# Kernel tuning notes

Measured on AMD Instinct MI355X. Metric: run time of the kernel, lower is better.

The kernel has to match this reference:

```python
import math
import jax, jax.numpy as jnp
import numpy as np

S, R, CM, CZ = 128, 256, 256, 128
H, C, PH, CT, FF = 8, 32, 4, 128, 4
SCALE = 1.0 / math.sqrt(C)


def _ln(x, w, b, eps=1e-5):
    mu = jnp.mean(x, axis=-1, keepdims=True)
    var = jnp.mean((x - mu) ** 2, axis=-1, keepdims=True)
    return (x - mu) * jax.lax.rsqrt(var + eps) * w + b


def _forward(msa, pair, rnm_w, rnm_b, r_gate, r_qkv, r_out, r_bias, cn_w, cn_b, c_gate, c_qkv, c_out, mtn_w, mtn_b, mt_p1, mt_p2, on_w, on_b, o_p1, o_p2, o_out, tmo_n1w, tmo_n1b, tmo_n2w, tmo_n2b, tmo_p1, tmo_p2, tmo_p3, tmo_p4, tmo_p5, tmo_p6, tmi_n1w, tmi_n1b, tmi_n2w, tmi_n2b, tmi_p1, tmi_p2, tmi_p3, tmi_p4, tmi_p5, tmi_p6, tas_nw, tas_nb, tas_gate, tas_qkv, tas_out, tas_bias, tae_nw, tae_nb, tae_gate, tae_qkv, tae_out, tae_bias, ptn_w, ptn_b, pt_p1, pt_p2):
    # --- MSA row attention with pair bias ---
    m = _ln(msa, rnm_w, rnm_b)
    q, k, v = jnp.split(m @ r_qkv, 3, axis=-1)
    q = q.reshape(S, R, H, C); k = k.reshape(S, R, H, C); v = v.reshape(S, R, H, C)
    bias = (pair @ r_bias).transpose(2, 0, 1)  # [H, i, j]
    logits = jnp.einsum('sihc,sjhc->shij', q, k) * SCALE + bias[None]
    o = jnp.einsum('shij,sjhc->sihc', jax.nn.softmax(logits, axis=-1), v).reshape(S, R, CM)
    msa = msa + (jax.nn.sigmoid(m @ r_gate) * o) @ r_out

    # --- MSA column attention (attend over sequence dim per residue) ---
    m = _ln(msa, cn_w, cn_b)
    q, k, v = jnp.split(m @ c_qkv, 3, axis=-1)
    q = q.reshape(S, R, H, C); k = k.reshape(S, R, H, C); v = v.reshape(S, R, H, C)
    logits = jnp.einsum('irhc,jrhc->hrij', q, k) * SCALE
    o = jnp.einsum('hrij,jrhc->irhc', jax.nn.softmax(logits, axis=-1), v).reshape(S, R, CM)
    msa = msa + (jax.nn.sigmoid(m @ c_gate) * o) @ c_out

    # --- MSA transition ---
    m = _ln(msa, mtn_w, mtn_b)
    msa = msa + jax.nn.relu(m @ mt_p1) @ mt_p2

    # --- Outer product mean ---
    m = _ln(msa, on_w, on_b)
    outer = jnp.einsum('sic,sjd->ijcd', m @ o_p1, m @ o_p2) / S
    pair = pair + outer.reshape(R, R, C * C) @ o_out

    # --- Triangle multiplicative update, outgoing (residual on normed pair, as in source) ---
    z = _ln(pair, tmo_n1w, tmo_n1b)
    left = (z @ tmo_p1) * jax.nn.sigmoid(z @ tmo_p2)
    right = (z @ tmo_p3) * jax.nn.sigmoid(z @ tmo_p4)
    g = jax.nn.sigmoid(z @ tmo_p6)
    x = _ln(jnp.einsum('ikc,jkc->ijc', left, right), tmo_n2w, tmo_n2b)
    pair = z + g * (x @ tmo_p5)

    # --- Triangle multiplicative update, incoming ---
    z = _ln(pair, tmi_n1w, tmi_n1b)
    left = (z @ tmi_p1) * jax.nn.sigmoid(z @ tmi_p2)
    right = (z @ tmi_p3) * jax.nn.sigmoid(z @ tmi_p4)
    g = jax.nn.sigmoid(z @ tmi_p6)
    x = _ln(jnp.einsum('kic,kjc->ijc', left, right), tmi_n2w, tmi_n2b)
    pair = z + g * (x @ tmi_p5)

    # --- Triangle attention, starting node: softmax over k of q_ij.k_ik + b_jk ---
    z = _ln(pair, tas_nw, tas_nb)
    b = (z @ tas_bias).transpose(2, 0, 1)  # [h, j, k]
    q, kk, v = jnp.split(z @ tas_qkv, 3, axis=-1)
    q = q.reshape(R, R, PH, C); kk = kk.reshape(R, R, PH, C); v = v.reshape(R, R, PH, C)
    logits = jnp.einsum('ijhc,ikhc->hijk', q, kk) * SCALE + b[:, None]
    o = jnp.einsum('hijk,ikhc->ijhc', jax.nn.softmax(logits, axis=-1), v).reshape(R, R, PH * C)
    pair = z + (jax.nn.sigmoid(z @ tas_gate) * o) @ tas_out

    # --- Triangle attention, ending node: softmax over k of q_ij.k_kj + b_ki ---
    z = _ln(pair, tae_nw, tae_nb)
    b = (z @ tae_bias).transpose(2, 1, 0)  # [h, i, k] = raw[k, i, h]
    q, kk, v = jnp.split(z @ tae_qkv, 3, axis=-1)
    q = q.reshape(R, R, PH, C); kk = kk.reshape(R, R, PH, C); v = v.reshape(R, R, PH, C)
    logits = jnp.einsum('ijhc,kjhc->hijk', q, kk) * SCALE + b[:, :, None, :]
    o = jnp.einsum('hijk,kjhc->ijhc', jax.nn.softmax(logits, axis=-1), v).reshape(R, R, PH * C)
    pair = z + (jax.nn.sigmoid(z @ tae_gate) * o) @ tae_out

    # --- Pair transition ---
    zt = _ln(pair, ptn_w, ptn_b)
    pair = pair + jax.nn.relu(zt @ pt_p1) @ pt_p2

    return (msa, pair)


def setup_inputs() -> dict:
    ks = iter(jax.random.split(jax.random.key(0), 80))
    def n(shape, s=1.0):
        return jax.random.normal(next(ks), shape, dtype=jnp.float32) * s
    w = lambda *shape: n(shape, 0.02)
    ones = lambda d: jnp.ones((d,), jnp.float32)
    zeros = lambda d: jnp.zeros((d,), jnp.float32)
    d = dict(
        msa=n((S, R, CM)), pair=n((R, R, CZ)),
        rnm_w=ones(CM), rnm_b=zeros(CM), r_gate=w(CM, CM), r_qkv=w(CM, 3 * CM), r_out=w(CM, CM), r_bias=w(CZ, H),
        cn_w=ones(CM), cn_b=zeros(CM), c_gate=w(CM, CM), c_qkv=w(CM, 3 * H * C), c_out=w(H * C, CM),
        mtn_w=ones(CM), mtn_b=zeros(CM), mt_p1=w(CM, FF * CM), mt_p2=w(FF * CM, CM),
        on_w=ones(CM), on_b=zeros(CM), o_p1=w(CM, C), o_p2=w(CM, C), o_out=w(C * C, CZ),
        tmo_n1w=ones(CZ), tmo_n1b=zeros(CZ), tmo_n2w=ones(CT), tmo_n2b=zeros(CT),
        tmo_p1=w(CZ, CT), tmo_p2=w(CZ, CT), tmo_p3=w(CZ, CT), tmo_p4=w(CZ, CT), tmo_p5=w(CT, CZ), tmo_p6=w(CZ, CZ),
        tmi_n1w=ones(CZ), tmi_n1b=zeros(CZ), tmi_n2w=ones(CT), tmi_n2b=zeros(CT),
        tmi_p1=w(CZ, CT), tmi_p2=w(CZ, CT), tmi_p3=w(CZ, CT), tmi_p4=w(CZ, CT), tmi_p5=w(CT, CZ), tmi_p6=w(CZ, CZ),
        tas_nw=ones(CZ), tas_nb=zeros(CZ), tas_gate=w(CZ, PH * C), tas_qkv=w(CZ, 3 * PH * C), tas_out=w(PH * C, CZ), tas_bias=w(CZ, PH),
        tae_nw=ones(CZ), tae_nb=zeros(CZ), tae_gate=w(CZ, PH * C), tae_qkv=w(CZ, 3 * PH * C), tae_out=w(PH * C, CZ), tae_bias=w(CZ, PH),
        ptn_w=ones(CZ), ptn_b=zeros(CZ), pt_p1=w(CZ, FF * CZ), pt_p2=w(FF * CZ, CZ),
    )
    return d


def reference(msa, pair, rnm_w, rnm_b, r_gate, r_qkv, r_out, r_bias, cn_w, cn_b, c_gate, c_qkv, c_out, mtn_w, mtn_b, mt_p1, mt_p2, on_w, on_b, o_p1, o_p2, o_out, tmo_n1w, tmo_n1b, tmo_n2w, tmo_n2b, tmo_p1, tmo_p2, tmo_p3, tmo_p4, tmo_p5, tmo_p6, tmi_n1w, tmi_n1b, tmi_n2w, tmi_n2b, tmi_p1, tmi_p2, tmi_p3, tmi_p4, tmi_p5, tmi_p6, tas_nw, tas_nb, tas_gate, tas_qkv, tas_out, tas_bias, tae_nw, tae_nb, tae_gate, tae_qkv, tae_out, tae_bias, ptn_w, ptn_b, pt_p1, pt_p2):
    return _forward(msa, pair, rnm_w, rnm_b, r_gate, r_qkv, r_out, r_bias, cn_w, cn_b, c_gate, c_qkv, c_out, mtn_w, mtn_b, mt_p1, mt_p2, on_w, on_b, o_p1, o_p2, o_out, tmo_n1w, tmo_n1b, tmo_n2w, tmo_n2b, tmo_p1, tmo_p2, tmo_p3, tmo_p4, tmo_p5, tmo_p6, tmi_n1w, tmi_n1b, tmi_n2w, tmi_n2b, tmi_p1, tmi_p2, tmi_p3, tmi_p4, tmi_p5, tmi_p6, tas_nw, tas_nb, tas_gate, tas_qkv, tas_out, tas_bias, tae_nw, tae_nb, tae_gate, tae_qkv, tae_out, tae_bias, ptn_w, ptn_b, pt_p1, pt_p2)
```

## Files before the change

### kernel.cpp

```cpp
#include <hip/hip_runtime.h>
#include <hip/hip_bf16.h>

typedef __hip_bfloat16 bf16;
typedef short v8s __attribute__((ext_vector_type(8)));
typedef float v4f __attribute__((ext_vector_type(4)));

#define SCALE_ 0.17677669529663687f
#define LOG2E_ 1.4426950408889634f

static __device__ __forceinline__ float sigf(float x){ return 1.f / (1.f + expf(-x)); }
static __device__ __forceinline__ float tof(float x){ return x; }
static __device__ __forceinline__ float tof(bf16 x){ return __bfloat162float(x); }
template<typename T> static __device__ __forceinline__ T fromf(float x);
template<> __device__ __forceinline__ float fromf<float>(float x){ return x; }
template<> __device__ __forceinline__ bf16  fromf<bf16 >(float x){ return __float2bfloat16(x); }
static __device__ __forceinline__ short b2s(float x){ bf16 b = __float2bfloat16(x); return *(short*)&b; }
static __device__ __forceinline__ float s2f(unsigned short s){ return __uint_as_float((unsigned)s << 16); }

static __device__ __forceinline__ void gload16(const void* g, void* l){
    __builtin_amdgcn_global_load_lds(
        (const __attribute__((address_space(1))) void*)g,
        (__attribute__((address_space(3))) void*)l,
        16, 0, 0);
}
static __device__ __forceinline__ v8s swzread(const short* S, int R, int l4){
    return *(const v8s*)&S[(R << 5) + (((l4) ^ (R & 3)) << 3)];
}

__global__ void detect_kernel(const unsigned short* w, int* flag){
    if (blockIdx.x == 0 && threadIdx.x == 0) flag[0] = (w[0] == 0x3F80) ? 0 : 1;
}
struct WC  { const void* s; bf16* d; int n; };
struct WC56 { WC w[56]; };
__global__ void cvtall_kernel(WC56 a, const int* flag){
    WC W = a.w[blockIdx.y];
    int i = blockIdx.x*256 + threadIdx.x;
    if (i >= W.n) return;
    float v = flag[0] ? ((const float*)W.s)[i] : tof(((const bf16*)W.s)[i]);
    W.d[i] = fromf<bf16>(v);
}
struct TC4 { const void* s; bf16* d; int K, N; };
struct TC34 { TC4 w[34]; };
__global__ void cvtTall_kernel(TC34 a, const int* flag){
    TC4 W = a.w[blockIdx.y];
    int idx = blockIdx.x*256 + threadIdx.x;
    if (idx >= W.K*W.N) return;
    int k = idx / W.N, n = idx - k*W.N;
    float v = flag[0] ? ((const float*)W.s)[idx] : tof(((const bf16*)W.s)[idx]);
    W.d[(size_t)n*W.K + k] = fromf<bf16>(v);
}
__global__ void cvt2f_kernel(const void* src, float* dst, int n4, const int* flag){
    int i = blockIdx.x*256 + threadIdx.x;
    if (i >= n4) return;
    if (flag[0]) ((float4*)dst)[i] = ((const float4*)src)[i];
    else {
        ushort4 v = ((const ushort4*)src)[i];
        float4 o;
        o.x = s2f(v.x); o.y = s2f(v.y); o.z = s2f(v.z); o.w = s2f(v.w);
        ((float4*)dst)[i] = o;
    }
}

template<typename TIN, typename TOUT, int D>
__global__ __launch_bounds__(256) void ln_kernel(const TIN* x, const bf16* w, const bf16* b, TOUT* y){
    constexpr int E = D/64;
    int wave = threadIdx.x >> 6, lane = threadIdx.x & 63;
    int row = blockIdx.x*4 + wave;
    size_t base = (size_t)row * D + lane*E;
    float v[E];
    if constexpr (sizeof(TIN)==4){
        if constexpr (E==4){ float4 t = *(const float4*)((const float*)x+base); v[0]=t.x;v[1]=t.y;v[2]=t.z;v[3]=t.w; }
        else { float2 t = *(const float2*)((const float*)x+base); v[0]=t.x;v[1]=t.y; }
    } else {
        if constexpr (E==4){ ushort4 t = *(const ushort4*)((const ushort*)x+base); v[0]=s2f(t.x);v[1]=s2f(t.y);v[2]=s2f(t.z);v[3]=s2f(t.w); }
        else { ushort2 t = *(const ushort2*)((const ushort*)x+base); v[0]=s2f(t.x);v[1]=s2f(t.y); }
    }
    float s1=0.f, s2=0.f;
    #pragma unroll
    for (int j=0;j<E;j++){ s1 += v[j]; s2 += v[j]*v[j]; }
    #pragma unroll
    for (int m=1;m<64;m<<=1){ s1 += __shfl_xor(s1,m,64); s2 += __shfl_xor(s2,m,64); }
    float mu  = s1*(1.0f/D);
    float var = s2*(1.0f/D) - mu*mu;
    float rs  = rsqrtf(fmaxf(var, 0.f) + 1e-5f);
    ushort wv[E], bw[E];
    if constexpr (E==4){ *(ushort4*)wv = *(const ushort4*)((const ushort*)w + lane*4);
                         *(ushort4*)bw = *(const ushort4*)((const ushort*)b + lane*4); }
    else               { *(ushort2*)wv = *(const ushort2*)((const ushort*)w + lane*2);
                         *(ushort2*)bw = *(const ushort2*)((const ushort*)b + lane*2); }
    ushort o[E];
    #pragma unroll
    for (int j=0;j<E;j++) o[j] = (ushort)b2s((v[j]-mu)*rs*s2f(wv[j]) + s2f(bw[j]));
    if constexpr (E==4) *(ushort4*)((ushort*)y + base) = *(ushort4*)o;
    else                *(ushort2*)((ushort*)y + base) = *(ushort2*)o;
}
template<int D>
__global__ __launch_bounds__(256) void ln2_kernel(const float* x, const bf16* w, const bf16* b, float* y, bf16* yB){
    constexpr int E = D/64;
    int wave = threadIdx.x >> 6, lane = threadIdx.x & 63;
    int row = blockIdx.x*4 + wave;
    size_t base = (size_t)row * D + lane*E;
    float2 t = *(const float2*)(x+base);
    float v0 = t.x, v1 = t.y;
    float s1 = v0+v1, s2 = v0*v0+v1*v1;
    #pragma unroll
    for (int m=1;m<64;m<<=1){ s1 += __shfl_xor(s1,m,64); s2 += __shfl_xor(s2,m,64); }
    float mu  = s1*(1.0f/D);
    float var = s2*(1.0f/D) - mu*mu;
    float rs  = rsqrtf(fmaxf(var, 0.f) + 1e-5f);
    ushort2 wv = *(const ushort2*)((const ushort*)w + lane*2);
    ushort2 bw = *(const ushort2*)((const ushort*)b + lane*2);
    float o0 = (v0-mu)*rs*s2f(wv.x) + s2f(bw.x);
    float o1 = (v1-mu)*rs*s2f(wv.y) + s2f(bw.y);
    float2 of; of.x = o0; of.y = o1;
    *(float2*)(y+base) = of;
    ushort ob[2]; ob[0] = (ushort)b2s(o0); ob[1] = (ushort)b2s(o1);
    *(ushort2*)((ushort*)yB + base) = *(ushort2*)ob;
}
__global__ __launch_bounds__(256) void lnT256_kernel(const float* x, const bf16* w, const bf16* b, bf16* y, bf16* yT){
    int wave = threadIdx.x >> 6, lane = threadIdx.x & 63;
    int row = blockIdx.x*4 + wave;
    int s = row >> 8, r = row & 255;
    size_t base = (size_t)row * 256 + lane*4;
    float4 t = *(const float4*)(x+base);
    float v[4] = {t.x, t.y, t.z, t.w};
    float s1=0.f, s2=0.f;
    #pragma unroll
    for (int j=0;j<4;j++){ s1 += v[j]; s2 += v[j]*v[j]; }
    #pragma unroll
    for (int m=1;m<64;m<<=1){ s1 += __shfl_xor(s1,m,64); s2 += __shfl_xor(s2,m,64); }
    float mu  = s1*(1.0f/256);
    float var = s2*(1.0f/256) - mu*mu;
    float rs  = rsqrtf(fmaxf(var, 0.f) + 1e-5f);
    ushort4 wv = *(const ushort4*)((const ushort*)w + lane*4);
    ushort4 bw = *(const ushort4*)((const ushort*)b + lane*4);
    ushort o[4];
    o[0] = (ushort)b2s((v[0]-mu)*rs*s2f(wv.x) + s2f(bw.x));
    o[1] = (ushort)b2s((v[1]-mu)*rs*s2f(wv.y) + s2f(bw.y));
    o[2] = (ushort)b2s((v[2]-mu)*rs*s2f(wv.z) + s2f(bw.z));
    o[3] = (ushort)b2s((v[3]-mu)*rs*s2f(wv.w) + s2f(bw.w));
    *(ushort4*)((ushort*)y + base) = *(ushort4*)o;
    *(ushort4*)((ushort*)yT + (((size_t)r << 7) + s)*256 + lane*4) = *(ushort4*)o;
}
__global__ __launch_bounds__(256) void ln2T128_kernel(const float* x, const bf16* w, const bf16* b,
                               float* y, bf16* yB, bf16* yT){
    int wave = threadIdx.x >> 6, lane = threadIdx.x & 63;
    int row = blockIdx.x*4 + wave;
    int i = row >> 8, j = row & 255;
    size_t base = (size_t)row * 128 + lane*2;
    float2 t = *(const float2*)(x+base);
    float v0 = t.x, v1 = t.y;
    float s1 = v0+v1, s2 = v0*v0+v1*v1;
    #pragma unroll
    for (int m=1;m<64;m<<=1){ s1 += __shfl_xor(s1,m,64); s2 += __shfl_xor(s2,m,64); }
    float mu  = s1*(1.0f/128);
    float var = s2*(1.0f/128) - mu*mu;
    float rs  = rsqrtf(fmaxf(var, 0.f) + 1e-5f);
    ushort2 wv = *(const ushort2*)((const ushort*)w + lane*2);
    ushort2 bw = *(const ushort2*)((const ushort*)b + lane*2);
    float o0 = (v0-mu)*rs*s2f(wv.x) + s2f(bw.x);
    float o1 = (v1-mu)*rs*s2f(wv.y) + s2f(bw.y);
    float2 of; of.x = o0; of.y = o1;
    *(float2*)(y+base) = of;
    ushort ob[2]; ob[0] = (ushort)b2s(o0); ob[1] = (ushort)b2s(o1);
    *(ushort2*)((ushort*)yB + base) = *(ushort2*)ob;
    *(ushort2*)((ushort*)yT + (((size_t)j << 8) + i)*128 + lane*2) = *(ushort2*)ob;
}

template<typename TC, typename TD>
__global__ __launch_bounds__(256) void mgemm_kernel(
    const bf16* A, const bf16* Wt, const TC* Cadd, TD* D,
    int M, int N, int K, int relu)
{
    __shared__ short As[4096];
    __shared__ short Bs[4096];
    int t = threadIdx.x;
    int wave = t >> 6, lane = t & 63;
    int wm = (wave >> 1) * 64, wn = (wave & 1) * 64;
    int m0 = blockIdx.y * 128, n0 = blockIdx.x * 128;
    const int l15 = lane & 15, l4 = lane >> 4;
    const int p0 = t, p1 = 256 + t;
    const int r0s = p0 >> 2, q0s = (p0 & 3) ^ (r0s & 3);
    const int r1s = p1 >> 2, q1s = (p1 & 3) ^ (r1s & 3);

// ... 30 lines not shown
            int col = n0 + wn + nf*16 + l15;
            #pragma unroll
            for (int r=0; r<4; r++){
                int row = r0 + r;
                float v = acc[mf][nf][r];
                if (Cadd) v += tof(Cadd[(size_t)row*N + col]);
                if (relu) v = fmaxf(v, 0.f);
                D[(size_t)row*N + col] = fromf<TD>(v);
            }
        }
    }
}

template<typename TA>
__global__ __launch_bounds__(256) void mgemm64_kernel(
    const TA* A, const bf16* Wt, bf16* D, int M, int N, int K)
{
    __shared__ short As[128][40];
    __shared__ short Bs[64][40];
    int t = threadIdx.x;
    int wave = t >> 6, lane = t & 63;
    int wm = (wave >> 1) * 64, wn = (wave & 1) * 32;
    int m0 = blockIdx.y * 128;
    int srow = t >> 1, skh = (t & 1) * 16;
    const int l15 = lane & 15, l4 = lane >> 4;

    v4f acc[4][2];
    #pragma unroll
    for (int i=0;i<4;i++){ acc[i][0] = (v4f)0.f; acc[i][1] = (v4f)0.f; }

    for (int k0 = 0; k0 < K; k0 += 32){
        if constexpr (sizeof(TA) == 2){
            const ushort* ag = (const ushort*)A + (size_t)(m0 + srow)*K + k0 + skh;
            *(uint4*)&As[srow][skh]     = *(const uint4*)(ag);
            *(uint4*)&As[srow][skh + 8] = *(const uint4*)(ag + 8);
        } else {
            const float* ap = (const float*)A + (size_t)(m0 + srow)*K + k0 + skh;
            #pragma unroll
            for (int q = 0; q < 4; q++){
                float4 v = *(const float4*)(ap + q*4);
                As[srow][skh+q*4+0] = b2s(v.x); As[srow][skh+q*4+1] = b2s(v.y);
                As[srow][skh+q*4+2] = b2s(v.z); As[srow][skh+q*4+3] = b2s(v.w);
            }
        }
        if (srow < 64){
            if (srow < N){
                const ushort* wg = (const ushort*)Wt + (size_t)srow*K + k0 + skh;
                *(uint4*)&Bs[srow][skh]     = *(const uint4*)(wg);
                *(uint4*)&Bs[srow][skh + 8] = *(const uint4*)(wg + 8);
            } else {
                uint4 z = {0,0,0,0};
                *(uint4*)&Bs[srow][skh] = z; *(uint4*)&Bs[srow][skh + 8] = z;
            }
        }
        __syncthreads();
        v8s af[4], bfr[2];
        #pragma unroll
        for (int mf=0; mf<4; mf++) af[mf] = *(const v8s*)&As[wm + mf*16 + l15][l4*8];
        #pragma unroll
        for (int nf=0; nf<2; nf++) bfr[nf] = *(const v8s*)&Bs[wn + nf*16 + l15][l4*8];
        #pragma unroll
        for (int mf=0; mf<4; mf++)
            #pragma unroll
            for (int nf=0; nf<2; nf++)
                acc[mf][nf] = __builtin_amdgcn_mfma_f32_16x16x32_bf16(
                    af[mf], bfr[nf], acc[mf][nf], 0, 0, 0);
        __syncthreads();
    }
    #pragma unroll
    for (int mf=0; mf<4; mf++){
        int r0 = m0 + wm + mf*16 + l4*4;
        #pragma unroll
        for (int nf=0; nf<2; nf++){
            int col = wn + nf*16 + l15;
            if (col < N){
                #pragma unroll
                for (int r=0; r<4; r++)
                    D[(size_t)(r0+r)*N + col] = fromf<bf16>(acc[mf][nf][r]);
            }
        }
    }
}

__global__ __launch_bounds__(256) void mgemm_opmA_kernel(
    const bf16* G, const bf16* Wt, const float* Cadd, float* D, int M, int N, int K)
{
    __shared__ short As[4096];
    __shared__ short Bs[4096];
    int t = threadIdx.x;
    int wave = t >> 6, lane = t & 63;
    int wm = (wave >> 1) * 64, wn = (wave & 1) * 64;
    int m0 = blockIdx.y * 128, n0 = blockIdx.x * 128;
    const int l15 = lane & 15, l4 = lane >> 4;
    const int p0 = t, p1 = 256 + t;
    const int r0s = p0 >> 2, q0s = (p0 & 3) ^ (r0s & 3);
    const int r1s = p1 >> 2, q1s = (p1 & 3) ^ (r1s & 3);
    const int ma = m0 + r0s, mb = m0 + r1s;

    v4f acc[4][4];
    #pragma unroll
    for (int i=0;i<4;i++)
        #pragma unroll
        for(int j=0;j<4;j++) acc[i][j] = (v4f)0.f;

    for (int k0 = 0; k0 < K; k0 += 32){
        int kb5 = k0 >> 5;
        gload16((const ushort*)G + ((size_t)((ma>>8)*32 + kb5))*8192 + (ma&255)*32 + q0s*8, &As[p0*8]);
        gload16((const ushort*)G + ((size_t)((mb>>8)*32 + kb5))*8192 + (mb&255)*32 + q1s*8, &As[p1*8]);
        gload16((const ushort*)Wt + (size_t)(n0 + r0s)*K + k0 + q0s*8, &Bs[p0*8]);
        gload16((const ushort*)Wt + (size_t)(n0 + r1s)*K + k0 + q1s*8, &Bs[p1*8]);
        __syncthreads();
        v8s af[4], bfr[4];
        #pragma unroll
        for (int mf=0; mf<4; mf++) af[mf]  = swzread(As, wm + mf*16 + l15, l4);
        #pragma unroll
        for (int nf=0; nf<4; nf++) bfr[nf] = swzread(Bs, wn + nf*16 + l15, l4);
        #pragma unroll
        for (int mf=0; mf<4; mf++)
            #pragma unroll
            for (int nf=0; nf<4; nf++)
                acc[mf][nf] = __builtin_amdgcn_mfma_f32_16x16x32_bf16(
                    af[mf], bfr[nf], acc[mf][nf], 0, 0, 0);
        __syncthreads();
    }
    #pragma unroll
    for (int mf=0; mf<4; mf++){
        int r0 = m0 + wm + mf*16 + l4*4;
        #pragma unroll
        for (int nf=0; nf<4; nf++){
            int col = n0 + wn + nf*16 + l15;
            #pragma unroll
            for (int r=0; r<4; r++){
                size_t idx = (size_t)(r0+r)*N + col;
                D[idx] = Cadd[idx] + acc[mf][nf][r];
            }
        }
    }
}

__global__ __launch_bounds__(256) void mgemm_gated_kernel(
    const bf16* G, const bf16* Oo, const bf16* Wt, const float* Cadd, float* D,
    int M, int N, int K)
{
    __shared__ short As[128][40];
    __shared__ short Bs[4096];
    int t = threadIdx.x;
    int wave = t >> 6, lane = t & 63;
    int wm = (wave >> 1) * 64, wn = (wave & 1) * 64;
    int m0 = blockIdx.y * 128, n0 = blockIdx.x * 128;
    int srow = t >> 1, skh = (t & 1) * 16;
    const int l15 = lane & 15, l4 = lane >> 4;
    const int p0 = t, p1 = 256 + t;
    const int r0s = p0 >> 2, q0s = (p0 & 3) ^ (r0s & 3);
    const int r1s = p1 >> 2, q1s = (p1 & 3) ^ (r1s & 3);

    v4f acc[4][4];
    #pragma unroll
    for (int i=0;i<4;i++)
        #pragma unroll
        for(int j=0;j<4;j++) acc[i][j] = (v4f)0.f;

    for (int k0 = 0; k0 < K; k0 += 32){
        gload16((const ushort*)Wt + (size_t)(n0 + r0s)*K + k0 + q0s*8, &Bs[p0*8]);
        gload16((const ushort*)Wt + (size_t)(n0 + r1s)*K + k0 + q1s*8, &Bs[p1*8]);
        const ushort* gg = (const ushort*)G  + (size_t)(m0 + srow)*K + k0 + skh;
        const ushort* oo = (const ushort*)Oo + (size_t)(m0 + srow)*K + k0 + skh;
        ushort ga[16], oa[16];
        *(uint4*)ga = *(const uint4*)gg;   *(uint4*)(ga+8) = *(const uint4*)(gg+8);
        *(uint4*)oa = *(const uint4*)oo;   *(uint4*)(oa+8) = *(const uint4*)(oo+8);
        #pragma unroll
        for (int j = 0; j < 16; j++)
            As[srow][skh + j] = b2s(s2f(oa[j]) * sigf(s2f(ga[j])));
        __syncthreads();
        v8s af[4], bfr[4];
        #pragma unroll
        for (int mf=0; mf<4; mf++) af[mf]  = *(const v8s*)&As[wm + mf*16 + l15][l4*8];
        #pragma unroll
        for (int nf=0; nf<4; nf++) bfr[nf] = swzread(Bs, wn + nf*16 + l15, l4);
        #pragma unroll
        for (int mf=0; mf<4; mf++)
            #pragma unroll
            for (int nf=0; nf<4; nf++)
                acc[mf][nf] = __builtin_amdgcn_mfma_f32_16x16x32_bf16(
                    af[mf], bfr[nf], acc[mf][nf], 0, 0, 0);
        __syncthreads();
    }
    #pragma unroll
    for (int mf=0; mf<4; mf++){
        int r0 = m0 + wm + mf*16 + l4*4;
        #pragma unroll
        for (int nf=0; nf<4; nf++){
            int col = n0 + wn + nf*16 + l15;
            #pragma unroll
            for (int r=0; r<4; r++){
                int row = r0 + r;
                float v = acc[mf][nf][r];
                if (Cadd) v += Cadd[(size_t)row*N + col];
                D[(size_t)row*N + col] = v;
            }
        }
    }
}

__global__ __launch_bounds__(256) void mgemm_glu_kernel(
    const bf16* A, const bf16* W1t, const bf16* W2t, bf16* D,
    int M, int N, int K)
{
    __shared__ short As[4096];
    __shared__ short B1s[4096];
    __shared__ short B2s[4096];
    int t = threadIdx.x;
    int wave = t >> 6, lane = t & 63;
    int wm = (wave >> 1) * 64, wn = (wave & 1) * 64;
    int m0 = blockIdx.y * 128, n0 = blockIdx.x * 128;
    const int l15 = lane & 15, l4 = lane >> 4;
    const int p0 = t, p1 = 256 + t;
    const int r0s = p0 >> 2, q0s = (p0 & 3) ^ (r0s & 3);
    const int r1s = p1 >> 2, q1s = (p1 & 3) ^ (r1s & 3);

    v4f acc1[4][4], acc2[4][4];
    #pragma unroll
    for (int i=0;i<4;i++)
        #pragma unroll
        for(int j=0;j<4;j++){ acc1[i][j] = (v4f)0.f; acc2[i][j] = (v4f)0.f; }

    for (int k0 = 0; k0 < K; k0 += 32){
        gload16((const ushort*)A   + (size_t)(m0 + r0s)*K + k0 + q0s*8, &As[p0*8]);
        gload16((const ushort*)A   + (size_t)(m0 + r1s)*K + k0 + q1s*8, &As[p1*8]);
        gload16((const ushort*)W1t + (size_t)(n0 + r0s)*K + k0 + q0s*8, &B1s[p0*8]);
        gload16((const ushort*)W1t + (size_t)(n0 + r1s)*K + k0 + q1s*8, &B1s[p1*8]);
        gload16((const ushort*)W2t + (size_t)(n0 + r0s)*K + k0 + q0s*8, &B2s[p0*8]);
        gload16((const ushort*)W2t + (size_t)(n0 + r1s)*K + k0 + q1s*8, &B2s[p1*8]);
        __syncthreads();
        v8s af[4], b1[4], b2[4];
        #pragma unroll
        for (int mf=0; mf<4; mf++) af[mf] = swzread(As, wm + mf*16 + l15, l4);
        #pragma unroll
        for (int nf=0; nf<4; nf++){
            b1[nf] = swzread(B1s, wn + nf*16 + l15, l4);
            b2[nf] = swzread(B2s, wn + nf*16 + l15, l4);
        }
        #pragma unroll
        for (int mf=0; mf<4; mf++)
            #pragma unroll
            for (int nf=0; nf<4; nf++){
                acc1[mf][nf] = __builtin_amdgcn_mfma_f32_16x16x32_bf16(af[mf], b1[nf], acc1[mf][nf], 0,0,0);
                acc2[mf][nf] = __builtin_amdgcn_mfma_f32_16x16x32_bf16(af[mf], b2[nf], acc2[mf][nf], 0,0,0);
            }
        __syncthreads();
    }
    #pragma unroll
    for (int mf=0; mf<4; mf++){
        int r0 = m0 + wm + mf*16 + l4*4;
        #pragma unroll
        for (int nf=0; nf<4; nf++){
            int col = n0 + wn + nf*16 + l15;
            #pragma unroll
            for (int r=0; r<4; r++)
                D[(size_t)(r0+r)*N + col] = fromf<bf16>(acc1[mf][nf][r] * sigf(acc2[mf][nf][r]));
        }
    }
}

__global__ __launch_bounds__(256) void mgemm_pairgate_kernel(
    const bf16* A, const bf16* Wt, const bf16* G, float* P,
    int M, int N, int K)
{
    __shared__ short As[4096];
    __shared__ short Bs[4096];
    int t = threadIdx.x;
    int wave = t >> 6, lane = t & 63;
    int wm = (wave >> 1) * 64, wn = (wave & 1) * 64;
    int m0 = blockIdx.y * 128, n0 = blockIdx.x * 128;
    const int l15 = lane & 15, l4 = lane >> 4;
    const int p0 = t, p1 = 256 + t;
    const int r0s = p0 >> 2, q0s = (p0 & 3) ^ (r0s & 3);
    const int r1s = p1 >> 2, q1s = (p1 & 3) ^ (r1s & 3);

    v4f acc[4][4];
    #pragma unroll
    for (int i=0;i<4;i++)
        #pragma unroll
        for(int j=0;j<4;j++) acc[i][j] = (v4f)0.f;

    for (int k0 = 0; k0 < K; k0 += 32){
        gload16((const ushort*)A  + (size_t)(m0 + r0s)*K + k0 + q0s*8, &As[p0*8]);
        gload16((const ushort*)A  + (size_t)(m0 + r1s)*K + k0 + q1s*8, &As[p1*8]);
        gload16((const ushort*)Wt + (size_t)(n0 + r0s)*K + k0 + q0s*8, &Bs[p0*8]);
        gload16((const ushort*)Wt + (size_t)(n0 + r1s)*K + k0 + q1s*8, &Bs[p1*8]);
        __syncthreads();
        v8s af[4], bfr[4];
        #pragma unroll
        for (int mf=0; mf<4; mf++) af[mf]  = swzread(As, wm + mf*16 + l15, l4);
        #pragma unroll
        for (int nf=0; nf<4; nf++) bfr[nf] = swzread(Bs, wn + nf*16 + l15, l4);
        #pragma unroll
        for (int mf=0; mf<4; mf++)
            #pragma unroll
            for (int nf=0; nf<4; nf++)
                acc[mf][nf] = __builtin_amdgcn_mfma_f32_16x16x32_bf16(
                    af[mf], bfr[nf], acc[mf][nf], 0, 0, 0);
        __syncthreads();
    }
    #pragma unroll
    for (int mf=0; mf<4; mf++){
        int r0 = m0 + wm + mf*16 + l4*4;
        #pragma unroll
        for (int nf=0; nf<4; nf++){
            int col = n0 + wn + nf*16 + l15;
            #pragma unroll
            for (int r=0; r<4; r++){
                size_t idx = (size_t)(r0+r)*N + col;
                P[idx] += sigf(tof(G[idx])) * acc[mf][nf][r];
            }
        }
    }
}

__global__ __launch_bounds__(256) void bmgemm_kernel(
    const bf16* A_, const bf16* Wt_, bf16* D_)
{
    const int K = 256, N = 256;
    const bf16* A  = A_  + (size_t)blockIdx.z*65536;
    const bf16* Wt = Wt_ + (size_t)blockIdx.z*65536;
    bf16*       D  = D_  + (size_t)blockIdx.z*65536;
    __shared__ short As[4096];
    __shared__ short Bs[4096];
    int t = threadIdx.x;
    int wave = t >> 6, lane = t & 63;
    int wm = (wave >> 1) * 64, wn = (wave & 1) * 64;
    int m0 = blockIdx.y * 128, n0 = blockIdx.x * 128;
    const int l15 = lane & 15, l4 = lane >> 4;
    const int p0 = t, p1 = 256 + t;
    const int r0s = p0 >> 2, q0s = (p0 & 3) ^ (r0s & 3);
    const int r1s = p1 >> 2, q1s = (p1 & 3) ^ (r1s & 3);

    v4f acc[4][4];
    #pragma unroll
    for (int i=0;i<4;i++)
        #pragma unroll
        for(int j=0;j<4;j++) acc[i][j] = (v4f)0.f;

// ... 84 lines not shown
        const ushort* bbase = (const ushort*)Bp + (size_t)h*65536;
        #pragma unroll
        for (int r = 0; r < 4; r++){
            const ushort* bp = bbase + (size_t)(q0 + wq + l4*4 + r)*256 + l15*16;
            *(uint4*)&bv[r][0] = *(const uint4*)(bp);
            *(uint4*)&bv[r][8] = *(const uint4*)(bp + 8);
        }
    }
    __syncthreads();

    v4f sacc[NF];
    #pragma unroll
    for (int f = 0; f < NF; f++){
        v8s bk_ = *(const v8s*)&Ks[(f*16+l15)*KST + l4*8];
        sacc[f] = __builtin_amdgcn_mfma_f32_16x16x32_bf16(aq, bk_, (v4f)0.f, 0, 0, 0);
    }
    float mrow[4] = {-3e38f,-3e38f,-3e38f,-3e38f};
    #pragma unroll
    for (int f = 0; f < NF; f++){
        #pragma unroll
        for (int r = 0; r < 4; r++){
            float v = sacc[f][r]*scale;
            if (Bp) v += s2f(bv[r][f]);
            sacc[f][r] = v;
            mrow[r] = fmaxf(mrow[r], v);
        }
    }
    #pragma unroll
    for (int m = 1; m < 16; m <<= 1){
        #pragma unroll
        for (int r = 0; r < 4; r++) mrow[r] = fmaxf(mrow[r], __shfl_xor(mrow[r], m, 64));
    }
    float srow[4] = {0.f,0.f,0.f,0.f};
    #pragma unroll
    for (int f = 0; f < NF; f++)
        #pragma unroll
        for (int r = 0; r < 4; r++){
            float e = exp2f(sacc[f][r] - mrow[r]);
            sacc[f][r] = e; srow[r] += e;
        }
    #pragma unroll
    for (int m = 1; m < 16; m <<= 1){
        #pragma unroll
        for (int r = 0; r < 4; r++) srow[r] += __shfl_xor(srow[r], m, 64);
    }
    float inv[4];
    #pragma unroll
    for (int r = 0; r < 4; r++) inv[r] = 1.f / srow[r];

    __syncthreads();
    const int PB = wave*16*PST;
    #pragma unroll
    for (int f = 0; f < NF; f++)
        #pragma unroll
        for (int r = 0; r < 4; r++)
            Ps[PB + (l4*4+r)*PST + f*16 + l15] = b2s(sacc[f][r]);
    v4f oacc0 = (v4f)0.f, oacc1 = (v4f)0.f;
    #pragma unroll
    for (int kk = 0; kk < KL; kk++){
        v8s ap   = *(const v8s*)&Ps[PB + l15*PST + kk*32 + l4*8];
        v8s bvv0 = *(const v8s*)&vbuf[l15*PST + kk*32 + l4*8];
        v8s bvv1 = *(const v8s*)&vbuf[(16+l15)*PST + kk*32 + l4*8];
        oacc0 = __builtin_amdgcn_mfma_f32_16x16x32_bf16(ap, bvv0, oacc0, 0, 0, 0);
        oacc1 = __builtin_amdgcn_mfma_f32_16x16x32_bf16(ap, bvv1, oacc1, 0, 0, 0);
    }
    #pragma unroll
    for (int r = 0; r < 4; r++){
        long long qg = q0 + wq + l4*4 + r;
        O[(long long)b*ob + qg*oq + h*32 + l15]      = fromf<bf16>(oacc0[r]*inv[r]);
        O[(long long)b*ob + qg*oq + h*32 + 16 + l15] = fromf<bf16>(oacc1[r]*inv[r]);
    }
}

__global__ void opm_T2_kernel(const bf16* src, bf16* aT, bf16* bT){
    int idx = blockIdx.x*256 + threadIdx.x;
    if (idx >= 2097152) return;
    int half = idx >> 20; int e = idx & 1048575;
    int s = e >> 13; int rem = e & 8191; int i = rem >> 5; int c = rem & 31;
    bf16 v = src[((size_t)s*256 + i)*64 + half*32 + c];
    if (half == 0) aT[((size_t)(i*32+c))*128 + s] = fromf<bf16>(tof(v) * (1.0f/128.0f));
    else           bT[((size_t)(i*32+c))*128 + s] = v;
}

__global__ __launch_bounds__(256) void triT_fwd_kernel(const bf16* in, bf16* out, int swap){
    __shared__ bf16 tile[32][34];
    int i  = blockIdx.z;
    int k0 = blockIdx.x*32;
    int c0 = blockIdx.y*32;
    int tx = threadIdx.x & 31, ty = threadIdx.x >> 5;
    for (int kk = ty; kk < 32; kk += 8){
        int k = k0+kk;
        size_t src = swap ? ((size_t)(k*256+i)*128 + c0+tx) : ((size_t)(i*256+k)*128 + c0+tx);
        tile[kk][tx] = in[src];
    }
    __syncthreads();
    for (int cc = ty; cc < 32; cc += 8){
        out[((size_t)(c0+cc)*256 + i)*256 + k0+tx] = tile[tx][cc];
    }
}
__global__ __launch_bounds__(256) void triT_bwd_kernel(const bf16* in, bf16* out){
    __shared__ bf16 tile[32][34];
    int i  = blockIdx.z;
    int j0 = blockIdx.x*32;
    int c0 = blockIdx.y*32;
    int tx = threadIdx.x & 31, ty = threadIdx.x >> 5;
    for (int cc = ty; cc < 32; cc += 8){
        tile[cc][tx] = in[((size_t)(c0+cc)*256 + i)*256 + j0+tx];
    }
    __syncthreads();
    for (int jj = ty; jj < 32; jj += 8){
        out[((size_t)i*256 + j0+jj)*128 + c0+tx] = tile[tx][jj];
    }
}

extern "C" void kernel_launch(void* const* d_in, const int* in_sizes, int n_in,
                              void* d_out, int out_size, void* d_ws, size_t ws_size,
                              hipStream_t stream) {
    (void)n_in; (void)out_size; (void)ws_size;
    const int NM = 8388608;
    const int NP = 8388608;

    float* msaF  = (float*)d_out;
    float* pairF = msaF + NM;

    char* w8 = (char*)d_ws;
    bf16*  B0 = (bf16*)(w8 + 0);
    bf16*  B1 = (bf16*)(w8 + 16777216);
    bf16*  B2 = (bf16*)(w8 + 33554432);
    bf16*  B5 = (bf16*)(w8 + 50331648);
    bf16*  B6 = (bf16*)(w8 + 67108864);
    bf16*  B4 = (bf16*)(w8 + 117440512);
    bf16*  BP = (bf16*)(w8 + 118489088);
    bf16*  Wb = (bf16*)(w8 + 119537664);
    bf16*  WtP= (bf16*)(w8 + 123731968);
    int*   flag = (int*)(w8 + 127926272);

    dim3 b256(256);
    auto nb = [](int n){ return (n + 255)/256; };
    const float SC2 = SCALE_ * LOG2E_;

    detect_kernel<<<1, 1, 0, stream>>>((const unsigned short*)d_in[2], flag);
    bf16* cw[58];
    WC56 wcArr;
    int maxN = 0;
    { size_t off = 0;
      for (int i = 2; i < 58; i++){
          cw[i] = Wb + off; off += (size_t)in_sizes[i];
          wcArr.w[i-2] = { d_in[i], cw[i], in_sizes[i] };
          if (in_sizes[i] > maxN) maxN = in_sizes[i];
      } }
    cvtall_kernel<<<dim3(nb(maxN), 56), b256, 0, stream>>>(wcArr, flag);

    struct TWh { int idx, K, N; };
    const TWh tw[34] = {{4,256,256},{5,256,768},{6,256,256},{7,128,8},
        {10,256,256},{11,256,768},{12,256,256},
        {15,256,1024},{16,1024,256},{19,256,32},{20,256,32},{21,1024,128},
        {26,128,128},{27,128,128},{28,128,128},{29,128,128},{30,128,128},{31,128,128},
        {36,128,128},{37,128,128},{38,128,128},{39,128,128},{40,128,128},{41,128,128},
        {44,128,128},{45,128,384},{46,128,128},{47,128,4},
        {50,128,128},{51,128,384},{52,128,128},{53,128,4},
        {56,128,512},{57,512,128}};
    bf16* cwT[58] = {};
    TC34 tcArr;
    int maxKN = 0;
    { size_t off = 0;
      for (int wi = 0; wi < 34; wi++){
          const TWh& w = tw[wi];
          cwT[w.idx] = WtP + off; off += (size_t)w.K * w.N;
          tcArr.w[wi] = { d_in[w.idx], cwT[w.idx], w.K, w.N };
          if (w.K*w.N > maxKN) maxKN = w.K*w.N;
      } }
    cvtTall_kernel<<<dim3(nb(maxKN), 34), b256, 0, stream>>>(tcArr, flag);

    cvt2f_kernel<<<nb(NM/4), b256, 0, stream>>>(d_in[0], msaF,  NM/4, flag);
    cvt2f_kernel<<<nb(NP/4), b256, 0, stream>>>(d_in[1], pairF, NP/4, flag);

    const bf16 *rnm_w=cw[2],  *rnm_b=cw[3];
    const bf16 *cn_w=cw[8],   *cn_b=cw[9];
    const bf16 *mtn_w=cw[13], *mtn_b=cw[14];
    const bf16 *on_w=cw[17],  *on_b=cw[18];
    const bf16 *tmo_n1w=cw[22],*tmo_n1b=cw[23],*tmo_n2w=cw[24],*tmo_n2b=cw[25];
    const bf16 *tmi_n1w=cw[32],*tmi_n1b=cw[33],*tmi_n2w=cw[34],*tmi_n2b=cw[35];
    const bf16 *tas_nw=cw[42],*tas_nb=cw[43];
    const bf16 *tae_nw=cw[48],*tae_nb=cw[49];
    const bf16 *ptn_w=cw[54], *ptn_b=cw[55];

    auto mg_b = [&](const bf16* A, const bf16* Wt, bf16* Dd, int M,int N,int K,int relu){
        dim3 g(N/128, M/128);
        mgemm_kernel<float,bf16><<<g, b256, 0, stream>>>(A, Wt, (const float*)nullptr, Dd, M,N,K,relu);
    };
    auto mg_f = [&](const bf16* A, const bf16* Wt, const float* Cs, float* Dd, int M,int N,int K){
        dim3 g(N/128, M/128);
        mgemm_kernel<float,float><<<g, b256, 0, stream>>>(A, Wt, Cs, Dd, M,N,K,0);
    };
    auto mg_gated = [&](const bf16* G, const bf16* Oo, const bf16* Wt, float* Dd, int M,int N,int K){
        dim3 g(N/128, M/128);
        mgemm_gated_kernel<<<g, b256, 0, stream>>>(G, Oo, Wt, Dd, Dd, M,N,K);
    };
    auto mg_glu = [&](const bf16* A, const bf16* W1, const bf16* W2, bf16* Dd, int M,int N,int K){
        dim3 g(N/128, M/128);
        mgemm_glu_kernel<<<g, b256, 0, stream>>>(A, W1, W2, Dd, M,N,K);
    };
    auto mg64_b = [&](const bf16* A, const bf16* Wt, bf16* Dd, int M,int N,int K){
        dim3 g(1, M/128);
        mgemm64_kernel<bf16><<<g, b256, 0, stream>>>(A, Wt, Dd, M,N,K);
    };
    auto mg64_f = [&](const float* A, const bf16* Wt, bf16* Dd, int M,int N,int K){
        dim3 g(1, M/128);
        mgemm64_kernel<float><<<g, b256, 0, stream>>>(A, Wt, Dd, M,N,K);
    };

    ln_kernel<float,bf16,256><<<8192, 256, 0, stream>>>(msaF, rnm_w, rnm_b, B0);
    mg_b(B0, cwT[4], B1, 32768, 256, 256, 0);
    mg64_f(pairF, cwT[7], B4, 65536, 8, 128);
    biasperm_kernel<<<nb(524288), b256, 0, stream>>>(B4, BP, 8, 0);
    mg_b(B0, cwT[5], B6, 32768, 768, 256, 0);
    fattn_kernel<256><<<dim3(128,8,4), b256, 0, stream>>>(
        B6, B6+256, B6+512, BP, B2,
        196608, 768, 196608, 768,  65536, 256, SC2);
    mg_gated(B1, B2, cwT[6], msaF, 32768, 256, 256);

    lnT256_kernel<<<8192, 256, 0, stream>>>(msaF, cn_w, cn_b, B0, B2);
    mg_b(B0, cwT[10], B1, 32768, 256, 256, 0);
    mg_b(B2, cwT[11], B6, 32768, 768, 256, 0);
    fattn_kernel<128><<<dim3(256,8,2), b256, 0, stream>>>(
        B6, B6+256, B6+512, nullptr, B0,
        98304, 768, 98304, 768,  256, 65536, SC2);
    mg_gated(B1, B0, cwT[12], msaF, 32768, 256, 256);

    ln_kernel<float,bf16,256><<<8192, 256, 0, stream>>>(msaF, mtn_w, mtn_b, B0);
    for (int q = 0; q < 2; q++){
        size_t off = (size_t)q * 16384 * 256;
        mg_b(B0 + off, cwT[15], B6, 16384, 1024, 256, 1);
        mg_f(B6, cwT[16], msaF + off, msaF + off, 16384, 256, 1024);
    }

    ln_kernel<float,bf16,256><<<8192, 256, 0, stream>>>(msaF, on_w, on_b, B0);
    mg64_b(B0, cwT[19], B1, 32768, 64, 256);
    opm_T2_kernel<<<nb(2097152), b256, 0, stream>>>(B1, B6, B6 + 1048576);
    for (int ic = 0; ic < 8; ic++){
        mg_b(B6 + (size_t)ic*131072, B6 + 1048576, B0, 1024, 8192, 128, 0);
        dim3 g(1, 64);
        mgemm_opmA_kernel<<<g, b256, 0, stream>>>(B0, cwT[21],
            pairF + (size_t)ic*1048576, pairF + (size_t)ic*1048576, 8192, 128, 1024);
    }

    ln2_kernel<128><<<16384, 256, 0, stream>>>(pairF, tmo_n1w, tmo_n1b, pairF, B5);
    mg_glu(B5, cwT[26], cwT[27], B2, 65536, 128, 128);
    mg_glu(B5, cwT[28], cwT[29], B0, 65536, 128, 128);
    triT_fwd_kernel<<<dim3(8,4,256), b256, 0, stream>>>(B2, B1, 0);
    triT_fwd_kernel<<<dim3(8,4,256), b256, 0, stream>>>(B0, B2, 0);
    bmgemm_kernel<<<dim3(2,2,128), b256, 0, stream>>>(B1, B2, B0);
    triT_bwd_kernel<<<dim3(8,4,256), b256, 0, stream>>>(B0, B1);
    ln_kernel<bf16,bf16,128><<<16384, 256, 0, stream>>>(B1, tmo_n2w, tmo_n2b, B1);
    mg_b(B5, cwT[31], B0, 65536, 128, 128, 0);
    { dim3 g(1, 512);
      mgemm_pairgate_kernel<<<g, b256, 0, stream>>>(B1, cwT[30], B0, pairF, 65536, 128, 128); }

    ln2_kernel<128><<<16384, 256, 0, stream>>>(pairF, tmi_n1w, tmi_n1b, pairF, B5);
    mg_glu(B5, cwT[36], cwT[37], B2, 65536, 128, 128);
    mg_glu(B5, cwT[38], cwT[39], B0, 65536, 128, 128);
    triT_fwd_kernel<<<dim3(8,4,256), b256, 0, stream>>>(B2, B1, 1);
    triT_fwd_kernel<<<dim3(8,4,256), b256, 0, stream>>>(B0, B2, 1);
    bmgemm_kernel<<<dim3(2,2,128), b256, 0, stream>>>(B1, B2, B0);
    triT_bwd_kernel<<<dim3(8,4,256), b256, 0, stream>>>(B0, B1);
    ln_kernel<bf16,bf16,128><<<16384, 256, 0, stream>>>(B1, tmi_n2w, tmi_n2b, B1);
    mg_b(B5, cwT[41], B0, 65536, 128, 128, 0);
    { dim3 g(1, 512);
      mgemm_pairgate_kernel<<<g, b256, 0, stream>>>(B1, cwT[40], B0, pairF, 65536, 128, 128); }

    ln2_kernel<128><<<16384, 256, 0, stream>>>(pairF, tas_nw, tas_nb, pairF, B5);
    mg64_b(B5, cwT[47], B4, 65536, 4, 128);
    biasperm_kernel<<<nb(262144), b256, 0, stream>>>(B4, BP, 4, 0);
    mg_b(B5, cwT[44], B1, 65536, 128, 128, 0);
    mg_b(B5, cwT[45], B6, 65536, 384, 128, 0);
    fattn_kernel<256><<<dim3(256,4,4), b256, 0, stream>>>(
        B6, B6+128, B6+256, BP, B2,
        98304, 384, 98304, 384,  32768, 128, SC2);
    mg_gated(B1, B2, cwT[46], pairF, 65536, 128, 128);

    ln2T128_kernel<<<16384, 256, 0, stream>>>(pairF, tae_nw, tae_nb, pairF, B5, B2);
    mg64_b(B5, cwT[53], B4, 65536, 4, 128);
    biasperm_kernel<<<nb(262144), b256, 0, stream>>>(B4, BP, 4, 1);
    mg_b(B5, cwT[50], B1, 65536, 128, 128, 0);
    mg_b(B2, cwT[51], B6, 65536, 384, 128, 0);
    fattn_kernel<256><<<dim3(256,4,4), b256, 0, stream>>>(
        B6, B6+128, B6+256, BP, B2,
        98304, 384, 98304, 384,  128, 32768, SC2);
    mg_gated(B1, B2, cwT[52], pairF, 65536, 128, 128);

    ln_kernel<float,bf16,128><<<16384, 256, 0, stream>>>(pairF, ptn_w, ptn_b, B0);
    for (int q = 0; q < 2; q++){
        size_t off = (size_t)q * 32768 * 128;
        mg_b(B0 + off, cwT[56], B6, 32768, 512, 128, 1);
        mg_f(B6, cwT[57], pairF + off, pairF + off, 32768, 128, 512);
    }
}
```

Baseline: 1.806 ms.

## Batch outer-product-mean and triangle GEMMs into fewer multi-job launches

The outer-product-mean chunk loop now issues its two GEMMs four chunks at a time through blockIdx.z, using four scratch buffers. The two GLU projections and the plain gate projection of each triangle update are merged into one three-job launch, and the two transposes are merged into one. This cuts kernel launch count and raises grid occupancy for small launches. The cost is extra scratch memory (B6 offsets) and per-block branching on job mode.

```diff
diff --git a/kernel.cpp b/kernel.cpp
--- a/kernel.cpp
+++ b/kernel.cpp
@@ -96,10 +96,9 @@
 }
 template<int D>
 __global__ __launch_bounds__(256) void ln2_kernel(const float* x, const bf16* w, const bf16* b, float* y, bf16* yB){
-    constexpr int E = D/64;
     int wave = threadIdx.x >> 6, lane = threadIdx.x & 63;
     int row = blockIdx.x*4 + wave;
-    size_t base = (size_t)row * D + lane*E;
+    size_t base = (size_t)row * D + lane*2;
     float2 t = *(const float2*)(x+base);
     float v0 = t.x, v1 = t.y;
     float s1 = v0+v1, s2 = v0*v0+v1*v1;
@@ -296,9 +295,68 @@
     }
 }
 
-__global__ __launch_bounds__(256) void mgemm_opmA_kernel(
-    const bf16* G, const bf16* Wt, const float* Cadd, float* D, int M, int N, int K)
+struct P4 { bf16* p[4]; };
+__global__ __launch_bounds__(256) void mgemm_opmG_kernel(
+    const bf16* aT, const bf16* bT, P4 dst, int icbase)
 {
+    const int N = 8192, K = 128;
+    const bf16* A = aT + (size_t)(icbase + blockIdx.z)*131072;
+    bf16* D = dst.p[blockIdx.z];
+    __shared__ short As[4096];
+    __shared__ short Bs[4096];
+    int t = threadIdx.x;
+    int wave = t >> 6, lane = t & 63;
+    int wm = (wave >> 1) * 64, wn = (wave & 1) * 64;
+    int m0 = blockIdx.y * 128, n0 = blockIdx.x * 128;
+    const int l15 = lane & 15, l4 = lane >> 4;
+    const int p0 = t, p1 = 256 + t;
+    const int r0s = p0 >> 2, q0s = (p0 & 3) ^ (r0s & 3);
+    const int r1s = p1 >> 2, q1s = (p1 & 3) ^ (r1s & 3);
+
+    v4f acc[4][4];
+    #pragma unroll
+    for (int i=0;i<4;i++)
+        #pragma unroll
+        for(int j=0;j<4;j++) acc[i][j] = (v4f)0.f;
+
+    for (int k0 = 0; k0 < K; k0 += 32){
+        gload16((const ushort*)A  + (size_t)(m0 + r0s)*K + k0 + q0s*8, &As[p0*8]);
+        gload16((const ushort*)A  + (size_t)(m0 + r1s)*K + k0 + q1s*8, &As[p1*8]);
+        gload16((const ushort*)bT + (size_t)(n0 + r0s)*K + k0 + q0s*8, &Bs[p0*8]);
+        gload16((const ushort*)bT + (size_t)(n0 + r1s)*K + k0 + q1s*8, &Bs[p1*8]);
+        __syncthreads();
+        v8s af[4], bfr[4];
+        #pragma unroll
+        for (int mf=0; mf<4; mf++) af[mf]  = swzread(As, wm + mf*16 + l15, l4);
+        #pragma unroll
+        for (int nf=0; nf<4; nf++) bfr[nf] = swzread(Bs, wn + nf*16 + l15, l4);
+        #pragma unroll
+        for (int mf=0; mf<4; mf++)
+            #pragma unroll
+            for (int nf=0; nf<4; nf++)
+                acc[mf][nf] = __builtin_amdgcn_mfma_f32_16x16x32_bf16(
+                    af[mf], bfr[nf], acc[mf][nf], 0, 0, 0);
+        __syncthreads();
+    }
+    #pragma unroll
+    for (int mf=0; mf<4; mf++){
+        int r0 = m0 + wm + mf*16 + l4*4;
+        #pragma unroll
+        for (int nf=0; nf<4; nf++){
+            int col = n0 + wn + nf*16 + l15;
+            #pragma unroll
+            for (int r=0; r<4; r++)
+                D[(size_t)(r0 + r)*N + col] = fromf<bf16>(acc[mf][nf][r]);
+        }
+    }
+}
+
+__global__ __launch_bounds__(256) void mgemm_opmA4_kernel(
+    P4 gsrc, const bf16* Wt, float* pairBase, int icbase)
+{
+    const int N = 128, K = 1024;
+    const bf16* G = gsrc.p[blockIdx.z];
+    float* D = pairBase + (size_t)(icbase + blockIdx.z)*1048576;
     __shared__ short As[4096];
     __shared__ short Bs[4096];
     int t = threadIdx.x;
@@ -346,7 +404,7 @@
             #pragma unroll
             for (int r=0; r<4; r++){
                 size_t idx = (size_t)(r0+r)*N + col;
-                D[idx] = Cadd[idx] + acc[mf][nf][r];
+                D[idx] = D[idx] + acc[mf][nf][r];
             }
         }
     }
@@ -416,13 +474,14 @@
     }
 }
 
-__global__ __launch_bounds__(256) void mgemm_glu_kernel(
-    const bf16* A, const bf16* W1t, const bf16* W2t, bf16* D,
-    int M, int N, int K)
+struct GluJob { const bf16* W1; const bf16* W2; bf16* D; int mode; };
+__global__ __launch_bounds__(256) void mgemm_glu3_kernel(
+    const bf16* A, GluJob j0, GluJob j1, GluJob j2, int M, int N, int K)
 {
     __shared__ short As[4096];
     __shared__ short B1s[4096];
     __shared__ short B2s[4096];
+    GluJob J = (blockIdx.z == 0) ? j0 : ((blockIdx.z == 1) ? j1 : j2);
     int t = threadIdx.x;
     int wave = t >> 6, lane = t & 63;
     int wm = (wave >> 1) * 64, wn = (wave & 1) * 64;
@@ -439,28 +498,35 @@
         for(int j=0;j<4;j++){ acc1[i][j] = (v4f)0.f; acc2[i][j] = (v4f)0.f; }
 
     for (int k0 = 0; k0 < K; k0 += 32){
-        gload16((const ushort*)A   + (size_t)(m0 + r0s)*K + k0 + q0s*8, &As[p0*8]);
-        gload16((const ushort*)A   + (size_t)(m0 + r1s)*K + k0 + q1s*8, &As[p1*8]);
-        gload16((const ushort*)W1t + (size_t)(n0 + r0s)*K + k0 + q0s*8, &B1s[p0*8]);
-        gload16((const ushort*)W1t + (size_t)(n0 + r1s)*K + k0 + q1s*8, &B1s[p1*8]);
-        gload16((const ushort*)W2t + (size_t)(n0 + r0s)*K + k0 + q0s*8, &B2s[p0*8]);
-        gload16((const ushort*)W2t + (size_t)(n0 + r1s)*K + k0 + q1s*8, &B2s[p1*8]);
-        __syncthreads();
-        v8s af[4], b1[4], b2[4];
+        gload16((const ushort*)A    + (size_t)(m0 + r0s)*K + k0 + q0s*8, &As[p0*8]);
+        gload16((const ushort*)A    + (size_t)(m0 + r1s)*K + k0 + q1s*8, &As[p1*8]);
+        gload16((const ushort*)J.W1 + (size_t)(n0 + r0s)*K + k0 + q0s*8, &B1s[p0*8]);
+        gload16((const ushort*)J.W1 + (size_t)(n0 + r1s)*K + k0 + q1s*8, &B1s[p1*8]);
+        if (J.mode == 0){
+            gload16((const ushort*)J.W2 + (size_t)(n0 + r0s)*K + k0 + q0s*8, &B2s[p0*8]);
+            gload16((const ushort*)J.W2 + (size_t)(n0 + r1s)*K + k0 + q1s*8, &B2s[p1*8]);
+        }
+        __syncthreads();
+        v8s af[4], b1[4];
         #pragma unroll
         for (int mf=0; mf<4; mf++) af[mf] = swzread(As, wm + mf*16 + l15, l4);
         #pragma unroll
-        for (int nf=0; nf<4; nf++){
-            b1[nf] = swzread(B1s, wn + nf*16 + l15, l4);
-            b2[nf] = swzread(B2s, wn + nf*16 + l15, l4);
-        }
+        for (int nf=0; nf<4; nf++) b1[nf] = swzread(B1s, wn + nf*16 + l15, l4);
         #pragma unroll
         for (int mf=0; mf<4; mf++)
             #pragma unroll
-            for (int nf=0; nf<4; nf++){
+            for (int nf=0; nf<4; nf++)
                 acc1[mf][nf] = __builtin_amdgcn_mfma_f32_16x16x32_bf16(af[mf], b1[nf], acc1[mf][nf], 0,0,0);
-                acc2[mf][nf] = __builtin_amdgcn_mfma_f32_16x16x32_bf16(af[mf], b2[nf], acc2[mf][nf], 0,0,0);
-            }
+        if (J.mode == 0){
+            v8s b2[4];
+            #pragma unroll
+            for (int nf=0; nf<4; nf++) b2[nf] = swzread(B2s, wn + nf*16 + l15, l4);
+            #pragma unroll
+            for (int mf=0; mf<4; mf++)
+                #pragma unroll
+                for (int nf=0; nf<4; nf++)
+                    acc2[mf][nf] = __builtin_amdgcn_mfma_f32_16x16x32_bf16(af[mf], b2[nf], acc2[mf][nf], 0,0,0);
+        }
         __syncthreads();
     }
     #pragma unroll
@@ -470,8 +536,11 @@
         for (int nf=0; nf<4; nf++){
             int col = n0 + wn + nf*16 + l15;
             #pragma unroll
-            for (int r=0; r<4; r++)
-                D[(size_t)(r0+r)*N + col] = fromf<bf16>(acc1[mf][nf][r] * sigf(acc2[mf][nf][r]));
+            for (int r=0; r<4; r++){
+                float v = acc1[mf][nf][r];
+                if (J.mode == 0) v *= sigf(acc2[mf][nf][r]);
+                J.D[(size_t)(r0+r)*N + col] = fromf<bf16>(v);
+            }
         }
     }
 }
@@ -722,9 +791,14 @@
     else           bT[((size_t)(i*32+c))*128 + s] = v;
 }
 
-__global__ __launch_bounds__(256) void triT_fwd_kernel(const bf16* in, bf16* out, int swap){
+__global__ __launch_bounds__(256) void triT_fwd2_kernel(
+    const bf16* in0, bf16* out0, const bf16* in1, bf16* out1, int swap)
+{
     __shared__ bf16 tile[32][34];
-    int i  = blockIdx.z;
+    int zz = blockIdx.z;
+    int i  = zz & 255;
+    const bf16* in = (zz < 256) ? in0 : in1;
+    bf16* out      = (zz < 256) ? out0 : out1;
     int k0 = blockIdx.x*32;
     int c0 = blockIdx.y*32;
     int tx = threadIdx.x & 31, ty = threadIdx.x >> 5;
@@ -837,10 +911,6 @@
         dim3 g(N/128, M/128);
         mgemm_gated_kernel<<<g, b256, 0, stream>>>(G, Oo, Wt, Dd, Dd, M,N,K);
     };
-    auto mg_glu = [&](const bf16* A, const bf16* W1, const bf16* W2, bf16* Dd, int M,int N,int K){
-        dim3 g(N/128, M/128);
-        mgemm_glu_kernel<<<g, b256, 0, stream>>>(A, W1, W2, Dd, M,N,K);
-    };
     auto mg64_b = [&](const bf16* A, const bf16* Wt, bf16* Dd, int M,int N,int K){
         dim3 g(1, M/128);
         mgemm64_kernel<bf16><<<g, b256, 0, stream>>>(A, Wt, Dd, M,N,K);
@@ -878,36 +948,35 @@
     ln_kernel<float,bf16,256><<<8192, 256, 0, stream>>>(msaF, on_w, on_b, B0);
     mg64_b(B0, cwT[19], B1, 32768, 64, 256);
     opm_T2_kernel<<<nb(2097152), b256, 0, stream>>>(B1, B6, B6 + 1048576);
-    for (int ic = 0; ic < 8; ic++){
-        mg_b(B6 + (size_t)ic*131072, B6 + 1048576, B0, 1024, 8192, 128, 0);
-        dim3 g(1, 64);
-        mgemm_opmA_kernel<<<g, b256, 0, stream>>>(B0, cwT[21],
-            pairF + (size_t)ic*1048576, pairF + (size_t)ic*1048576, 8192, 128, 1024);
-    }
+    { P4 g; g.p[0] = B0; g.p[1] = B1; g.p[2] = B2; g.p[3] = B5;
+      for (int icb = 0; icb < 8; icb += 4){
+          mgemm_opmG_kernel<<<dim3(64,8,4), b256, 0, stream>>>(B6, B6 + 1048576, g, icb);
+          mgemm_opmA4_kernel<<<dim3(1,64,4), b256, 0, stream>>>(g, cwT[21], pairF, icb);
+      } }
 
     ln2_kernel<128><<<16384, 256, 0, stream>>>(pairF, tmo_n1w, tmo_n1b, pairF, B5);
-    mg_glu(B5, cwT[26], cwT[27], B2, 65536, 128, 128);
-    mg_glu(B5, cwT[28], cwT[29], B0, 65536, 128, 128);
-    triT_fwd_kernel<<<dim3(8,4,256), b256, 0, stream>>>(B2, B1, 0);
-    triT_fwd_kernel<<<dim3(8,4,256), b256, 0, stream>>>(B0, B2, 0);
-    bmgemm_kernel<<<dim3(2,2,128), b256, 0, stream>>>(B1, B2, B0);
+    { GluJob j0 = {cwT[26], cwT[27], B2, 0};
+      GluJob j1 = {cwT[28], cwT[29], B0, 0};
+      GluJob j2 = {cwT[31], cwT[31], B6, 1};
+      mgemm_glu3_kernel<<<dim3(1,512,3), b256, 0, stream>>>(B5, j0, j1, j2, 65536, 128, 128); }
+    triT_fwd2_kernel<<<dim3(8,4,512), b256, 0, stream>>>(B2, B1, B0, B6 + 8388608, 0);
+    bmgemm_kernel<<<dim3(2,2,128), b256, 0, stream>>>(B1, B6 + 8388608, B0);
     triT_bwd_kernel<<<dim3(8,4,256), b256, 0, stream>>>(B0, B1);
     ln_kernel<bf16,bf16,128><<<16384, 256, 0, stream>>>(B1, tmo_n2w, tmo_n2b, B1);
-    mg_b(B5, cwT[31], B0, 65536, 128, 128, 0);
     { dim3 g(1, 512);
-      mgemm_pairgate_kernel<<<g, b256, 0, stream>>>(B1, cwT[30], B0, pairF, 65536, 128, 128); }
+      mgemm_pairgate_kernel<<<g, b256, 0, stream>>>(B1, cwT[30], B6, pairF, 65536, 128, 128); }
 
     ln2_kernel<128><<<16384, 256, 0, stream>>>(pairF, tmi_n1w, tmi_n1b, pairF, B5);
-    mg_glu(B5, cwT[36], cwT[37], B2, 65536, 128, 128);
-    mg_glu(B5, cwT[38], cwT[39], B0, 65536, 128, 128);
-    triT_fwd_kernel<<<dim3(8,4,256), b256, 0, stream>>>(B2, B1, 1);
-    triT_fwd_kernel<<<dim3(8,4,256), b256, 0, stream>>>(B0, B2, 1);
-    bmgemm_kernel<<<dim3(2,2,128), b256, 0, stream>>>(B1, B2, B0);
+    { GluJob j0 = {cwT[36], cwT[37], B2, 0};
+      GluJob j1 = {cwT[38], cwT[39], B0, 0};
+      GluJob j2 = {cwT[41], cwT[41], B6, 1};
+      mgemm_glu3_kernel<<<dim3(1,512,3), b256, 0, stream>>>(B5, j0, j1, j2, 65536, 128, 128); }
+    triT_fwd2_kernel<<<dim3(8,4,512), b256, 0, stream>>>(B2, B1, B0, B6 + 8388608, 1);
+    bmgemm_kernel<<<dim3(2,2,128), b256, 0, stream>>>(B1, B6 + 8388608, B0);
     triT_bwd_kernel<<<dim3(8,4,256), b256, 0, stream>>>(B0, B1);
     ln_kernel<bf16,bf16,128><<<16384, 256, 0, stream>>>(B1, tmi_n2w, tmi_n2b, B1);
-    mg_b(B5, cwT[41], B0, 65536, 128, 128, 0);
     { dim3 g(1, 512);
-      mgemm_pairgate_kernel<<<g, b256, 0, stream>>>(B1, cwT[40], B0, pairF, 65536, 128, 128); }
+      mgemm_pairgate_kernel<<<g, b256, 0, stream>>>(B1, cwT[40], B6, pairF, 65536, 128, 128); }
 
     ln2_kernel<128><<<16384, 256, 0, stream>>>(pairF, tas_nw, tas_nb, pairF, B5);
     mg64_b(B5, cwT[47], B4, 65536, 4, 128);
```

Result: faster. 1.494 ms (-17.3%).
